# Optimization experiments

Hardware: AMD Instinct MI355X
Metric: run time of the kernel (lower is better)

Reference implementation:

```python
import jax, jax.numpy as jnp
import numpy as np

N_IN, D_IN, N_OUT, D_OUT = 1152, 8, 10, 16
ROUTINGS, NUM_BG = 3, 1
C, H, W = 1, 28, 28
BATCH = 128
DEC_IN = N_OUT * D_OUT  # 160, projection_type=None -> dec_feature_size = outcaps_size


def squash(x, axis=-1):
    norm = jnp.linalg.norm(x, axis=axis, keepdims=True)
    scale = norm ** 2 / (1.0 + norm ** 2) / (norm + 1e-8)
    return scale * x


def scale_coef(x, num_bg):
    # x: [B, n_out] or [B, n_out, n_in]; min/max normalize over dim 1,
    # excluding the last num_bg (background) capsules, then floor at 0.5.
    if num_bg > 0:
        xm = x[:, : x.shape[1] - num_bg]
    else:
        xm = x
    mn = jnp.min(xm, axis=1, keepdims=True)
    mx = jnp.max(xm, axis=1, keepdims=True)
    out = (xm - mn) / jnp.maximum(mx - mn, 1e-6)  # vrange (0,1)
    if num_bg > 0:
        out = jnp.concatenate([out, jnp.zeros_like(out[:, :num_bg])], axis=1)
    return jnp.maximum(out, 0.5)


def decode(capsflat, W1, b1, W2, b2, W3, b3):
    # fcn decoder (eval mode: dropout is identity): 160 -> 512 -> 1024 -> C*H*W
    h = jax.nn.relu(capsflat @ W1 + b1)
    h = jax.nn.relu(h @ W2 + b2)
    return jax.nn.sigmoid(h @ W3 + b3)


def setup_inputs() -> dict:
    key = jax.random.key(0)
    ks = jax.random.split(key, 9)
    return {
        'incaps': jax.random.normal(ks[0], (BATCH, N_IN, D_IN), jnp.float32),
        'x_input': jax.random.uniform(ks[1], (BATCH, C, H, W), jnp.float32),
        'weight': 0.1 * jax.random.normal(ks[2], (N_OUT, N_IN, D_OUT, D_IN), jnp.float32),
        'W1': 0.05 * jax.random.normal(ks[3], (DEC_IN, 512), jnp.float32),
        'b1': jnp.zeros((512,), jnp.float32),
        'W2': 0.05 * jax.random.normal(ks[4], (512, 1024), jnp.float32),
        'b2': jnp.zeros((1024,), jnp.float32),
        'W3': 0.05 * jax.random.normal(ks[5], (1024, C * H * W), jnp.float32),
        'b3': jnp.zeros((C * H * W,), jnp.float32),
    }


def reference(incaps, x_input, weight, W1, b1, W2, b2, W3, b3):
    B = incaps.shape[0]
    # outcaps_hat: matmul(weight, incaps[:,None,:,:,None]).squeeze(-1)
    hat = jnp.einsum('nkoi,bki->bnko', weight, incaps)  # [B, n_out, n_in, d_out]
    hat_d = jax.lax.stop_gradient(hat)
    rc = jnp.ones((B, N_OUT, N_IN), hat.dtype)
    eye = jnp.eye(N_OUT, dtype=hat.dtype)
    x_flat = x_input.reshape(B, 1, -1)
    for _ in range(ROUTINGS - 1):
        # squash over capsule dim, weighted sum over input capsules
        outcaps = squash(jnp.sum(rc[..., None] * hat_d, axis=2, keepdims=True))  # [B,n,1,d]
        b = jnp.sum(outcaps * hat_d, axis=-1)  # agreement [B, n_out, n_in]
        c = scale_coef(b, NUM_BG)
        objcaps = outcaps[:, :, 0, :]  # [B, n_out, d_out]
        # get_every_obj_rscore vectorized: mask one object capsule at a time
        masked = objcaps[:, None, :, :] * eye[None, :, :, None]  # [B, n_obj, n_out, d]
        recon = decode(masked.reshape(B, N_OUT, DEC_IN), W1, b1, W2, b2, W3, b3)  # [B,n_obj,CHW]
        rscore = -jnp.sum((x_flat - recon) ** 2, axis=-1)  # neg MSE-sum, [B, n_obj]
        r = scale_coef(rscore, NUM_BG)
        rc = c * r[:, :, None]
    # final iteration uses non-detached hat
    outcaps = squash(jnp.sum(rc[..., None] * hat, axis=2, keepdims=True))
    return outcaps[:, :, 0, :]  # [B, n_out, d_out]
```

## Files before the change

kernel.cpp:

```cpp
#include <hip/hip_runtime.h>
#include <math.h>

#define BATCH  128
#define NIN    1152
#define DIN    8
#define NOUTC  10
#define DOUT   16
#define H1DIM  512
#define H2DIM  1024
#define PIX    784
#define NROWS  (BATCH * NOUTC)
#define NBY3   13

typedef __attribute__((ext_vector_type(8))) __bf16 bf16x8;
typedef __attribute__((ext_vector_type(4))) float  f32x4;
typedef __attribute__((ext_vector_type(4))) unsigned int u32x4;

__device__ __forceinline__ float bf2f(unsigned int u) {
    union { unsigned int i; float f; } v; v.i = u << 16; return v.f;
}
__device__ __forceinline__ ushort f2bf(float f) {
    union { float f; unsigned int i; } v; v.f = f;
    unsigned int r = v.i + 0x7FFFu + ((v.i >> 16) & 1u);
    return (ushort)(r >> 16);
}
__device__ __forceinline__ float ldin(const void* p, size_t i, int isbf) {
    return isbf ? bf2f(((const ushort*)p)[i]) : ((const float*)p)[i];
}
__device__ __forceinline__ bf16x8 frag_of(uint4 u) {
    return __builtin_bit_cast(bf16x8, u);
}
__device__ __forceinline__ bf16x8 ld_frag(const ushort* p) {
    return frag_of(*(const uint4*)p);
}
__device__ __forceinline__ float dot8(uint4 a, uint4 b) {
    float s;
    s  = bf2f(a.x & 0xffffu) * bf2f(b.x & 0xffffu);
    s += bf2f(a.x >> 16)     * bf2f(b.x >> 16);
    s += bf2f(a.y & 0xffffu) * bf2f(b.y & 0xffffu);
    s += bf2f(a.y >> 16)     * bf2f(b.y >> 16);
    s += bf2f(a.z & 0xffffu) * bf2f(b.z & 0xffffu);
    s += bf2f(a.z >> 16)     * bf2f(b.z >> 16);
    s += bf2f(a.w & 0xffffu) * bf2f(b.w & 0xffffu);
    s += bf2f(a.w >> 16)     * bf2f(b.w >> 16);
    return s;
}
__device__ __forceinline__ uint4 pack8(float4 a, float4 b) {
    uint4 r;
    r.x = f2bf(a.x) | ((unsigned)f2bf(a.y) << 16);
    r.y = f2bf(a.z) | ((unsigned)f2bf(a.w) << 16);
    r.z = f2bf(b.x) | ((unsigned)f2bf(b.y) << 16);
    r.w = f2bf(b.z) | ((unsigned)f2bf(b.w) << 16);
    return r;
}

__device__ __forceinline__ int detect_bf(const void* w, int* cntS) {
    int tid = threadIdx.x, nt = blockDim.x;
    if (tid == 0) *cntS = 0;
    __syncthreads();
    const ushort* u = (const ushort*)w;
    int c = 0;
    for (int s = tid; s < 512; s += nt) {
        int e = (u[s * 2] >> 7) & 0xFF;
        if (e >= 88 && e <= 140) c++;
    }
    atomicAdd(cntS, c);
    __syncthreads();
    return (*cntS >= 384) ? 1 : 0;
}

struct PrepArgs {
    const void* w;
    const void* src[7];
    ushort*     dst[7];
    int         n[7];
    int*        flag;
};

__global__ __launch_bounds__(256) void prep_kernel(PrepArgs a)
{
    __shared__ int cntS;
    __shared__ ushort tile[32][33];
    int tid = threadIdx.x;
    int isbf = detect_bf(a.w, &cntS);
    int seg = blockIdx.y;
    if (seg == 0 && blockIdx.x == 0 && tid == 0) *a.flag = isbf;

    if (seg <= 4) {
        int n = a.n[seg];
        int stride = gridDim.x * 256;
        ushort* d = a.dst[seg];
        if (isbf) {
            const ushort* s = (const ushort*)a.src[seg];
            for (int i = blockIdx.x * 256 + tid; i < n; i += stride) d[i] = s[i];
        } else {
            const float* s = (const float*)a.src[seg];
            for (int i = blockIdx.x * 256 + tid; i < n; i += stride) d[i] = f2bf(s[i]);
        }
        return;
    }
    int R = (seg == 5) ? H1DIM : H2DIM;
    int C = (seg == 5) ? H2DIM : PIX;
    int tilesX = (seg == 5) ? 32 : 25;
    int tilesY = (seg == 5) ? 16 : 32;
    int t = blockIdx.x;
    if (t >= tilesX * tilesY) return;
    int tx2 = t % tilesX, ty2 = t / tilesX;
    int c0 = tx2 * 32, r0 = ty2 * 32;
    const void* in = a.src[seg];
    ushort* out = a.dst[seg];
    int tx = tid & 31, ty = tid >> 5;
    for (int i = ty; i < 32; i += 8) {
        int r = r0 + i, c = c0 + tx;
        tile[i][tx] = (r < R && c < C) ? f2bf(ldin(in, (size_t)r * C + c, isbf)) : (ushort)0;
    }
    __syncthreads();
    for (int i = ty; i < 32; i += 8) {
        int c = c0 + i, r = r0 + tx;
        if (c < C && r < R) out[(size_t)c * R + r] = tile[tx][i];
    }
}

__global__ __launch_bounds__(256) void hat_build(
    const void* __restrict__ inc,
    const void* __restrict__ w,
    ushort* __restrict__ hatG)
{
    __shared__ int cntS;
    int isbf = detect_bf(w, &cntS);
    int kc = blockIdx.x, bc = blockIdx.y, n = blockIdx.z;
    int t  = threadIdx.x;
    int k  = kc * 128 + (t >> 1);
    int oh = (t & 1) << 3;

    size_t wbase = ((size_t)n * NIN + k) * DOUT + oh;
    uint4 wr[8];
    if (isbf) {
        const uint4* wp = (const uint4*)((const ushort*)w + wbase * DIN);
        #pragma unroll
        for (int j = 0; j < 8; j++) wr[j] = wp[j];
    } else {
        const float4* wp = (const float4*)((const float*)w + wbase * DIN);
        #pragma unroll
        for (int j = 0; j < 8; j++) wr[j] = pack8(wp[2 * j], wp[2 * j + 1]);
    }

    int b0 = bc * 16;
    #pragma unroll 4
    for (int bl = 0; bl < 16; bl++) {
        int b = b0 + bl;
        size_t ioff = ((size_t)b * NIN + k) * DIN;
        uint4 iu;
        if (isbf) iu = *(const uint4*)((const ushort*)inc + ioff);
        else {
            const float4* ip = (const float4*)((const float*)inc + ioff);
            iu = pack8(ip[0], ip[1]);
        }
        unsigned int h[8];
        #pragma unroll
        for (int j = 0; j < 8; j++) h[j] = f2bf(dot8(wr[j], iu));
        u32x4 ov = { h[0] | (h[1] << 16), h[2] | (h[3] << 16),
                     h[4] | (h[5] << 16), h[6] | (h[7] << 16) };
        __builtin_nontemporal_store(ov,
            (u32x4*)(hatG + (((size_t)(b * NOUTC + n) * NIN + k) * DOUT + oh)));
    }
}

template<bool COMPUTE>
__global__ __launch_bounds__(512, 4) void reduce_pass(
    const ushort* __restrict__ hatG,
    const void*   __restrict__ incRaw,
    const void*   __restrict__ wRaw,
    const ushort* __restrict__ bsPrev,
    const float*  __restrict__ partials,
    int iter0,
    const ushort* __restrict__ W1c,
    const ushort* __restrict__ b1c,
    ushort* __restrict__ h1out,
    ushort* __restrict__ bsOut,
    void*   __restrict__ outFinal,
    const int* __restrict__ flagp)
{
    int bn  = blockIdx.x;
    int n   = bn % NOUTC;
    int b   = bn / NOUTC;
    int tid = threadIdx.x;

    __shared__ ushort wSb[NIN];
    __shared__ float  redS[8][16];
    __shared__ float  sumS[16];
    __shared__ float  ocS[16];
    __shared__ float  scaleS;

    int h = tid & 1, kb = tid >> 1;
    int wave = tid >> 6, lane = tid & 63;

    uint4 v[4];
    const ushort* tailS;

    if constexpr (!COMPUTE) {
        __shared__ uint4 hatTail4[256];
        const ushort* hbase = hatG + (size_t)bn * NIN * DOUT;
        #pragma unroll
        for (int j = 0; j < 4; j++)
            v[j] = *(const uint4*)(hbase + ((kb + 256 * j) * DOUT + h * 8));
        if (tid < 256)
            hatTail4[tid] = *(const uint4*)(hbase + 1024 * DOUT + tid * 8);
        tailS = (const ushort*)hatTail4;
    } else {
        __shared__ int cntS;
        __shared__ uint4 hatS4[NIN * DOUT / 8];
        int isbf = detect_bf(wRaw, &cntS);
        size_t wnb = (size_t)n * NIN * DOUT * DIN;
        for (int idx = tid; idx < NIN * DOUT; idx += 512) {
            int k = idx >> 4;
            float s = 0.f;
            #pragma unroll
            for (int i = 0; i < 8; i++)
                s += ldin(wRaw, wnb + (size_t)idx * 8 + i, isbf) *
                     ldin(incRaw, ((size_t)b * NIN + k) * DIN + i, isbf);
            ((ushort*)hatS4)[idx] = f2bf(s);
        }
        __syncthreads();
        const ushort* hbase = (const ushort*)hatS4;
        #pragma unroll
        for (int j = 0; j < 4; j++)
            v[j] = *(const uint4*)(hbase + ((kb + 256 * j) * DOUT + h * 8));
        tailS = hbase + 1024 * DOUT;
    }

    if (!iter0) {
        if (tid < 9) {
            float s = 0.f;
            #pragma unroll
            for (int j = 0; j < NBY3; j++)
                s += partials[(size_t)(b * NOUTC + tid) * 16 + j];
            sumS[tid] = -s;
        }
        __syncthreads();
        float mn = 1e30f, mx = -1e30f;
        #pragma unroll
        for (int n2 = 0; n2 < 9; n2++) {
            float vv = sumS[n2];
            mn = fminf(mn, vv); mx = fmaxf(mx, vv);
        }
        float den = fmaxf(mx - mn, 1e-6f);
        float rv = (n < 9) ? fmaxf((sumS[n] - mn) / den, 0.5f) : 0.5f;
        for (int k = tid; k < NIN; k += 512) {
            float c = 0.5f;
            if (n < 9) {
                float vv[9], mn2 = 1e30f, mx2 = -1e30f;
                #pragma unroll
                for (int n2 = 0; n2 < 9; n2++) {
                    vv[n2] = bf2f(bsPrev[(size_t)(b * NOUTC + n2) * NIN + k]);
                    mn2 = fminf(mn2, vv[n2]); mx2 = fmaxf(mx2, vv[n2]);
                }
                float den2 = fmaxf(mx2 - mn2, 1e-6f);
                c = fmaxf((vv[n] - mn2) / den2, 0.5f);
            }
            wSb[k] = f2bf(c * rv);
        }
    }
    __syncthreads();

    float acc[8];
    #pragma unroll
    for (int o = 0; o < 8; o++) acc[o] = 0.f;
    #pragma unroll
    for (int j = 0; j < 4; j++) {
        int k = kb + 256 * j;
        float w = iter0 ? 1.f : bf2f(wSb[k]);
        bf16x8 hv = frag_of(v[j]);
        #pragma unroll
        for (int o = 0; o < 8; o++) acc[o] += w * (float)hv[o];
    }
    if (tid < 256) {
        int k = 1024 + kb;
        float w = iter0 ? 1.f : bf2f(wSb[k]);
        bf16x8 hv = ld_frag(tailS + kb * DOUT + h * 8);
        #pragma unroll
        for (int o = 0; o < 8; o++) acc[o] += w * (float)hv[o];
    }
    #pragma unroll
    for (int off = 32; off >= 2; off >>= 1) {
        #pragma unroll
        for (int o = 0; o < 8; o++) acc[o] += __shfl_xor(acc[o], off);
    }
    if (lane < 2) {
        #pragma unroll
        for (int o = 0; o < 8; o++) redS[wave][lane * 8 + o] = acc[o];
    }
    __syncthreads();
    if (tid < 16) {
        float s = 0.f;
        #pragma unroll
        for (int wv = 0; wv < 8; wv++) s += redS[wv][tid];
        sumS[tid] = s;
    }
    __syncthreads();
    if (tid == 0) {
        float n2 = 0.f;
        #pragma unroll
        for (int o = 0; o < 16; o++) n2 += sumS[o] * sumS[o];
        float nrm = sqrtf(n2);
        scaleS = n2 / (1.f + n2) / (nrm + 1e-8f);
    }
    __syncthreads();
    if (tid < 16) {
        float oc = scaleS * sumS[tid];
        ocS[tid] = oc;
        if (outFinal) {
            if (*flagp) ((ushort*)outFinal)[(size_t)bn * 16 + tid] = f2bf(oc);
            else        ((float*) outFinal)[(size_t)bn * 16 + tid] = oc;
        }
    }
    __syncthreads();

    if (bsOut) {
        float o0 = ocS[h * 8 + 0], o1 = ocS[h * 8 + 1], o2 = ocS[h * 8 + 2],
              o3 = ocS[h * 8 + 3], o4 = ocS[h * 8 + 4], o5 = ocS[h * 8 + 5],
              o6 = ocS[h * 8 + 6], o7 = ocS[h * 8 + 7];
        #pragma unroll
        for (int j = 0; j < 4; j++) {
            bf16x8 hv = frag_of(v[j]);
            float s = o0 * (float)hv[0] + o1 * (float)hv[1] + o2 * (float)hv[2] +
                      o3 * (float)hv[3] + o4 * (float)hv[4] + o5 * (float)hv[5] +
                      o6 * (float)hv[6] + o7 * (float)hv[7];
            s += __shfl_xor(s, 1);
            if (h == 0) bsOut[(size_t)bn * NIN + kb + 256 * j] = f2bf(s);
        }
        if (tid < 256) {
            bf16x8 hv = ld_frag(tailS + kb * DOUT + h * 8);
            float s = o0 * (float)hv[0] + o1 * (float)hv[1] + o2 * (float)hv[2] +
                      o3 * (float)hv[3] + o4 * (float)hv[4] + o5 * (float)hv[5] +
                      o6 * (float)hv[6] + o7 * (float)hv[7];
            s += __shfl_xor(s, 1);
            if (h == 0) bsOut[(size_t)bn * NIN + 1024 + kb] = f2bf(s);
        }
    }

    if (h1out) {
        int col = tid;
        float acc1 = bf2f(b1c[col]);
        #pragma unroll
        for (int i = 0; i < 16; i++)
            acc1 += ocS[i] * bf2f(W1c[(size_t)(n * 16 + i) * H1DIM + col]);
        h1out[(size_t)bn * H1DIM + col] = f2bf(fmaxf(acc1, 0.f));
    }
}

__global__ __launch_bounds__(256) void gemm_kernel(
    const ushort* __restrict__ A, const ushort* __restrict__ Bt,
    const ushort* __restrict__ bias, int K, int N,
    ushort* __restrict__ Cout,
    const ushort* __restrict__ xin, float* __restrict__ partials)
{
    int m0 = blockIdx.x * 64, n0 = blockIdx.y * 64;
    int tid = threadIdx.x;
    int wave = tid >> 6, lane = tid & 63, quad = lane >> 4, l16 = lane & 15;

    __shared__ uint4 As4[320];
    __shared__ uint4 Bs4[320];
    ushort* As = (ushort*)As4;
    ushort* Bs = (ushort*)Bs4;

    f32x4 acc[4];
    #pragma unroll
    for (int nt = 0; nt < 4; nt++)
        #pragma unroll
        for (int rg = 0; rg < 4; rg++) acc[nt][rg] = 0.f;

    int sMi = tid >> 2, sKk = (tid & 3) * 8;
    int sLds = sMi * 5 + (tid & 3);
    const ushort* Ap = A + (size_t)(m0 + sMi) * K + sKk;
    const ushort* Bp = Bt + (size_t)(n0 + sMi) * K + sKk;
    bool bOK = (n0 + sMi) < N;

    uint4 aR = *(const uint4*)Ap;
    uint4 bR = bOK ? *(const uint4*)Bp : make_uint4(0, 0, 0, 0);

    for (int k0 = 0; k0 < K; k0 += 32) {
        As4[sLds] = aR;
        Bs4[sLds] = bR;
        __syncthreads();
        if (k0 + 32 < K) {
            aR = *(const uint4*)(Ap + k0 + 32);
            bR = bOK ? *(const uint4*)(Bp + k0 + 32) : make_uint4(0, 0, 0, 0);
        }
        bf16x8 a = ld_frag(As + (wave * 16 + l16) * 40 + quad * 8);
        #pragma unroll
        for (int nt = 0; nt < 4; nt++) {
            bf16x8 bb = ld_frag(Bs + (nt * 16 + l16) * 40 + quad * 8);
            acc[nt] = __builtin_amdgcn_mfma_f32_16x16x32_bf16(a, bb, acc[nt], 0, 0, 0);
        }
        __syncthreads();
    }

    int rowBase = m0 + wave * 16 + quad * 4;
    if (Cout) {
        #pragma unroll
        for (int nt = 0; nt < 4; nt++) {
            int col = n0 + nt * 16 + l16;
            float bv = bf2f(bias[col]);
            #pragma unroll
            for (int rg = 0; rg < 4; rg++) {
                float v = acc[nt][rg] + bv;
                Cout[(size_t)(rowBase + rg) * N + col] = f2bf(fmaxf(v, 0.f));
            }
        }
    } else {
        float vr[4] = {0.f, 0.f, 0.f, 0.f};
        #pragma unroll
        for (int nt = 0; nt < 4; nt++) {
            int col = n0 + nt * 16 + l16;
            if (col < N) {
                float bv = bf2f(bias[col]);
                #pragma unroll
                for (int rg = 0; rg < 4; rg++) {
                    int row = rowBase + rg;
                    int bb = row / NOUTC;
                    float z = acc[nt][rg] + bv;
                    float s = 1.f / (1.f + __expf(-z));
                    float d = bf2f(xin[(size_t)bb * PIX + col]) - s;
                    vr[rg] += d * d;
                }
            }
        }
        #pragma unroll
        for (int rg = 0; rg < 4; rg++) {
            float v = vr[rg];
            #pragma unroll
            for (int off = 8; off >= 1; off >>= 1) v += __shfl_xor(v, off, 16);
            if (l16 == 0)
                partials[(size_t)(rowBase + rg) * 16 + blockIdx.y] = v;
        }
    }
}

extern "C" void kernel_launch(void* const* d_in, const int* in_sizes, int n_in,
                              void* d_out, int out_size, void* d_ws, size_t ws_size,
                              hipStream_t stream)
{
    const void* inc = d_in[0];
    const void* x   = d_in[1];
    const void* w   = d_in[2];
    const void* W1  = d_in[3];
    const void* b1  = d_in[4];
    const void* W2  = d_in[5];
    const void* b2  = d_in[6];
    const void* W3  = d_in[7];
    const void* b3  = d_in[8];

    char* p = (char*)d_ws;
    auto alloc = [&](size_t bytes) { void* r = p; p += (bytes + 255) & ~(size_t)255; return r; };
    int*    flagWS    = (int*)alloc(256);
    ushort* bsA       = (ushort*)alloc((size_t)NROWS * NIN * 2);
    ushort* bsB       = (ushort*)alloc((size_t)NROWS * NIN * 2);
    float*  partials  = (float*)alloc((size_t)NROWS * 16 * 4);
    ushort* h1WS      = (ushort*)alloc((size_t)NROWS * H1DIM * 2);
    ushort* h2WS      = (ushort*)alloc((size_t)NROWS * H2DIM * 2);
    ushort* W2T       = (ushort*)alloc((size_t)H2DIM * H1DIM * 2);
    ushort* W3T       = (ushort*)alloc((size_t)PIX * H2DIM * 2);
    ushort* W1c       = (ushort*)alloc((size_t)160 * H1DIM * 2);
    ushort* b1c       = (ushort*)alloc((size_t)H1DIM * 2);
    ushort* b2c       = (ushort*)alloc((size_t)H2DIM * 2);
    ushort* b3c       = (ushort*)alloc((size_t)PIX * 2);
    ushort* xc        = (ushort*)alloc((size_t)BATCH * PIX * 2);
    ushort* hatG      = (ushort*)alloc((size_t)NROWS * NIN * DOUT * 2);
    bool haveHat = ((char*)hatG + (size_t)NROWS * NIN * DOUT * 2) <= ((char*)d_ws + ws_size);

    PrepArgs pa;
    pa.w = w;
    pa.src[0] = W1;  pa.dst[0] = W1c;  pa.n[0] = 160 * H1DIM;
    pa.src[1] = b1;  pa.dst[1] = b1c;  pa.n[1] = H1DIM;
    pa.src[2] = b2;  pa.dst[2] = b2c;  pa.n[2] = H2DIM;
    pa.src[3] = b3;  pa.dst[3] = b3c;  pa.n[3] = PIX;
    pa.src[4] = x;   pa.dst[4] = xc;   pa.n[4] = BATCH * PIX;
    pa.src[5] = W2;  pa.dst[5] = W2T;  pa.n[5] = 0;
    pa.src[6] = W3;  pa.dst[6] = W3T;  pa.n[6] = 0;
    pa.flag = flagWS;
    prep_kernel<<<dim3(800, 7), 256, 0, stream>>>(pa);

    if (haveHat) hat_build<<<dim3(9, 8, NOUTC), 256, 0, stream>>>(inc, w, hatG);

    if (haveHat)
        reduce_pass<false><<<NROWS, 512, 0, stream>>>(
            hatG, inc, w, nullptr, nullptr, 1,
            W1c, b1c, h1WS, bsA, nullptr, flagWS);
    else
        reduce_pass<true><<<NROWS, 512, 0, stream>>>(
            nullptr, inc, w, nullptr, nullptr, 1,
            W1c, b1c, h1WS, bsA, nullptr, flagWS);

    for (int it = 0; it < 2; it++) {
        gemm_kernel<<<dim3(NROWS / 64, H2DIM / 64), 256, 0, stream>>>(
            h1WS, W2T, b2c, H1DIM, H2DIM, h2WS, nullptr, nullptr);
        gemm_kernel<<<dim3(NROWS / 64, NBY3), 256, 0, stream>>>(
            h2WS, W3T, b3c, H2DIM, PIX, nullptr, xc, partials);

        int last = (it == 1);
        const ushort* bsP = (it == 0) ? bsA : bsB;
        ushort* bsO       = last ? nullptr : bsB;
        ushort* h1o       = last ? nullptr : h1WS;
        void*   fin       = last ? d_out : nullptr;
        if (haveHat)
            reduce_pass<false><<<NROWS, 512, 0, stream>>>(
                hatG, inc, w, bsP, partials, 0,
                W1c, b1c, h1o, bsO, fin, flagWS);
        else
            reduce_pass<true><<<NROWS, 512, 0, stream>>>(
                nullptr, inc, w, bsP, partials, 0,
                W1c, b1c, h1o, bsO, fin, flagWS);
    }
}
```

Baseline: 214.1 us.

## Fuse weight prep into hat build, use fp32 hat math, double GEMM k-step

Merges the separate prep kernel into the hat-building kernel by appending extra grid slices that perform the weight transposes, bias/input conversions and flag write, which removes one kernel launch. The hat computation now unpacks weights and inputs to fp32 once instead of re-converting bf16 in every dot product. The GEMM stages two 32-wide k-chunks per barrier pair to halve synchronisation, at the cost of doubling shared memory. The 96 transpose blocks each loop over about 14 tiles, which may lengthen the critical path of the fused kernel.

```diff
diff --git a/kernel.cpp b/kernel.cpp
--- a/kernel.cpp
+++ b/kernel.cpp
@@ -33,17 +33,11 @@
 __device__ __forceinline__ bf16x8 ld_frag(const ushort* p) {
     return frag_of(*(const uint4*)p);
 }
-__device__ __forceinline__ float dot8(uint4 a, uint4 b) {
-    float s;
-    s  = bf2f(a.x & 0xffffu) * bf2f(b.x & 0xffffu);
-    s += bf2f(a.x >> 16)     * bf2f(b.x >> 16);
-    s += bf2f(a.y & 0xffffu) * bf2f(b.y & 0xffffu);
-    s += bf2f(a.y >> 16)     * bf2f(b.y >> 16);
-    s += bf2f(a.z & 0xffffu) * bf2f(b.z & 0xffffu);
-    s += bf2f(a.z >> 16)     * bf2f(b.z >> 16);
-    s += bf2f(a.w & 0xffffu) * bf2f(b.w & 0xffffu);
-    s += bf2f(a.w >> 16)     * bf2f(b.w >> 16);
-    return s;
+__device__ __forceinline__ void unpack8(uint4 u, float* f) {
+    f[0] = bf2f(u.x & 0xffffu); f[1] = bf2f(u.x >> 16);
+    f[2] = bf2f(u.y & 0xffffu); f[3] = bf2f(u.y >> 16);
+    f[4] = bf2f(u.z & 0xffffu); f[5] = bf2f(u.z >> 16);
+    f[6] = bf2f(u.w & 0xffffu); f[7] = bf2f(u.w >> 16);
 }
 __device__ __forceinline__ uint4 pack8(float4 a, float4 b) {
     uint4 r;
@@ -121,44 +115,104 @@
     }
 }
 
-__global__ __launch_bounds__(256) void hat_build(
+__global__ __launch_bounds__(256) void hat_prep_kernel(
     const void* __restrict__ inc,
-    const void* __restrict__ w,
+    PrepArgs a,
     ushort* __restrict__ hatG)
 {
     __shared__ int cntS;
-    int isbf = detect_bf(w, &cntS);
+    __shared__ ushort tile[32][33];
+    int tid = threadIdx.x;
+    int isbf = detect_bf(a.w, &cntS);
+
+    if (blockIdx.z >= NOUTC) {
+        int p = (blockIdx.z - NOUTC) * 72 + blockIdx.y * 9 + blockIdx.x;
+        if (p == 0 && tid == 0) *a.flag = isbf;
+        if (p < 96) {
+            for (int t = p; t < 1312; t += 96) {
+                int seg = (t < 512) ? 5 : 6;
+                int tt  = (seg == 5) ? t : t - 512;
+                int R = (seg == 5) ? H1DIM : H2DIM;
+                int C = (seg == 5) ? H2DIM : PIX;
+                int tilesX = (seg == 5) ? 32 : 25;
+                int tx2 = tt % tilesX, ty2 = tt / tilesX;
+                int c0 = tx2 * 32, r0 = ty2 * 32;
+                const void* in = a.src[seg];
+                ushort* out = a.dst[seg];
+                int tx = tid & 31, ty = tid >> 5;
+                for (int i = ty; i < 32; i += 8) {
+                    int r = r0 + i, c = c0 + tx;
+                    tile[i][tx] = (r < R && c < C) ? f2bf(ldin(in, (size_t)r * C + c, isbf)) : (ushort)0;
+                }
+                __syncthreads();
+                for (int i = ty; i < 32; i += 8) {
+                    int c = c0 + i, r = r0 + tx;
+                    if (c < C && r < R) out[(size_t)c * R + r] = tile[tx][i];
+                }
+                __syncthreads();
+            }
+        } else {
+            int base = (p - 96) * 256 + tid;
+            const int stride = 48 * 256;
+            #pragma unroll
+            for (int seg = 0; seg <= 4; seg++) {
+                int n = a.n[seg];
+                ushort* d = a.dst[seg];
+                if (isbf) {
+                    const ushort* s = (const ushort*)a.src[seg];
+                    for (int i = base; i < n; i += stride) d[i] = s[i];
+                } else {
+                    const float* s = (const float*)a.src[seg];
+                    for (int i = base; i < n; i += stride) d[i] = f2bf(s[i]);
+                }
+            }
+        }
+        return;
+    }
+
     int kc = blockIdx.x, bc = blockIdx.y, n = blockIdx.z;
-    int t  = threadIdx.x;
-    int k  = kc * 128 + (t >> 1);
-    int oh = (t & 1) << 3;
+    int k  = kc * 128 + (tid >> 1);
+    int oh = (tid & 1) << 3;
 
     size_t wbase = ((size_t)n * NIN + k) * DOUT + oh;
-    uint4 wr[8];
+    float wf[8][8];
     if (isbf) {
-        const uint4* wp = (const uint4*)((const ushort*)w + wbase * DIN);
-        #pragma unroll
-        for (int j = 0; j < 8; j++) wr[j] = wp[j];
+        const uint4* wp = (const uint4*)((const ushort*)a.w + wbase * DIN);
+        #pragma unroll
+        for (int j = 0; j < 8; j++) unpack8(wp[j], wf[j]);
     } else {
-        const float4* wp = (const float4*)((const float*)w + wbase * DIN);
-        #pragma unroll
-        for (int j = 0; j < 8; j++) wr[j] = pack8(wp[2 * j], wp[2 * j + 1]);
+        const float4* wp = (const float4*)((const float*)a.w + wbase * DIN);
+        #pragma unroll
+        for (int j = 0; j < 8; j++) {
+            float4 lo = wp[2 * j], hi = wp[2 * j + 1];
+            wf[j][0] = lo.x; wf[j][1] = lo.y; wf[j][2] = lo.z; wf[j][3] = lo.w;
+            wf[j][4] = hi.x; wf[j][5] = hi.y; wf[j][6] = hi.z; wf[j][7] = hi.w;
+        }
     }
 
     int b0 = bc * 16;
-    #pragma unroll 4
+    #pragma unroll 2
     for (int bl = 0; bl < 16; bl++) {
         int b = b0 + bl;
         size_t ioff = ((size_t)b * NIN + k) * DIN;
-        uint4 iu;
-        if (isbf) iu = *(const uint4*)((const ushort*)inc + ioff);
-        else {
+        float xi[8];
+        if (isbf) {
+            uint4 iu = *(const uint4*)((const ushort*)inc + ioff);
+            unpack8(iu, xi);
+        } else {
             const float4* ip = (const float4*)((const float*)inc + ioff);
-            iu = pack8(ip[0], ip[1]);
+            float4 lo = ip[0], hi = ip[1];
+            xi[0] = lo.x; xi[1] = lo.y; xi[2] = lo.z; xi[3] = lo.w;
+            xi[4] = hi.x; xi[5] = hi.y; xi[6] = hi.z; xi[7] = hi.w;
         }
         unsigned int h[8];
         #pragma unroll
-        for (int j = 0; j < 8; j++) h[j] = f2bf(dot8(wr[j], iu));
+        for (int j = 0; j < 8; j++) {
+            float s = wf[j][0] * xi[0] + wf[j][1] * xi[1] + wf[j][2] * xi[2] +
+                      wf[j][3] * xi[3] + wf[j][4] * xi[4] + wf[j][5] * xi[5] +
+                      wf[j][6] * xi[6] + wf[j][7] * xi[7];
+            h[j] = f2bf(s);
+        }
         u32x4 ov = { h[0] | (h[1] << 16), h[2] | (h[3] << 16),
                      h[4] | (h[5] << 16), h[6] | (h[7] << 16) };
         __builtin_nontemporal_store(ov,
@@ -359,8 +413,8 @@
     int tid = threadIdx.x;
     int wave = tid >> 6, lane = tid & 63, quad = lane >> 4, l16 = lane & 15;
 
-    __shared__ uint4 As4[320];
-    __shared__ uint4 Bs4[320];
+    __shared__ uint4 As4[640];
+    __shared__ uint4 Bs4[640];
     ushort* As = (ushort*)As4;
     ushort* Bs = (ushort*)Bs4;
 
@@ -376,22 +430,31 @@
     const ushort* Bp = Bt + (size_t)(n0 + sMi) * K + sKk;
     bool bOK = (n0 + sMi) < N;
 
-    uint4 aR = *(const uint4*)Ap;
-    uint4 bR = bOK ? *(const uint4*)Bp : make_uint4(0, 0, 0, 0);
-
-    for (int k0 = 0; k0 < K; k0 += 32) {
-        As4[sLds] = aR;
-        Bs4[sLds] = bR;
+    uint4 aR0 = *(const uint4*)Ap;
+    uint4 aR1 = *(const uint4*)(Ap + 32);
+    uint4 bR0 = bOK ? *(const uint4*)Bp : make_uint4(0, 0, 0, 0);
+    uint4 bR1 = bOK ? *(const uint4*)(Bp + 32) : make_uint4(0, 0, 0, 0);
+
+    for (int k0 = 0; k0 < K; k0 += 64) {
+        As4[sLds]       = aR0;
+        As4[320 + sLds] = aR1;
+        Bs4[sLds]       = bR0;
+        Bs4[320 + sLds] = bR1;
         __syncthreads();
-        if (k0 + 32 < K) {
-            aR = *(const uint4*)(Ap + k0 + 32);
-            bR = bOK ? *(const uint4*)(Bp + k0 + 32) : make_uint4(0, 0, 0, 0);
-        }
-        bf16x8 a = ld_frag(As + (wave * 16 + l16) * 40 + quad * 8);
-        #pragma unroll
-        for (int nt = 0; nt < 4; nt++) {
-            bf16x8 bb = ld_frag(Bs + (nt * 16 + l16) * 40 + quad * 8);
-            acc[nt] = __builtin_amdgcn_mfma_f32_16x16x32_bf16(a, bb, acc[nt], 0, 0, 0);
+        if (k0 + 64 < K) {
+            aR0 = *(const uint4*)(Ap + k0 + 64);
+            aR1 = *(const uint4*)(Ap + k0 + 96);
+            bR0 = bOK ? *(const uint4*)(Bp + k0 + 64) : make_uint4(0, 0, 0, 0);
+            bR1 = bOK ? *(const uint4*)(Bp + k0 + 96) : make_uint4(0, 0, 0, 0);
+        }
+        #pragma unroll
+        for (int c = 0; c < 2; c++) {
+            bf16x8 a = ld_frag(As + c * 2560 + (wave * 16 + l16) * 40 + quad * 8);
+            #pragma unroll
+            for (int nt = 0; nt < 4; nt++) {
+                bf16x8 bb = ld_frag(Bs + c * 2560 + (nt * 16 + l16) * 40 + quad * 8);
+                acc[nt] = __builtin_amdgcn_mfma_f32_16x16x32_bf16(a, bb, acc[nt], 0, 0, 0);
+            }
         }
         __syncthreads();
     }
@@ -479,9 +542,12 @@
     pa.src[5] = W2;  pa.dst[5] = W2T;  pa.n[5] = 0;
     pa.src[6] = W3;  pa.dst[6] = W3T;  pa.n[6] = 0;
     pa.flag = flagWS;
-    prep_kernel<<<dim3(800, 7), 256, 0, stream>>>(pa);
-
-    if (haveHat) hat_build<<<dim3(9, 8, NOUTC), 256, 0, stream>>>(inc, w, hatG);
+
+    if (haveHat) {
+        hat_prep_kernel<<<dim3(9, 8, NOUTC + 2), 256, 0, stream>>>(inc, pa, hatG);
+    } else {
+        prep_kernel<<<dim3(800, 7), 256, 0, stream>>>(pa);
+    }
 
     if (haveHat)
         reduce_pass<false><<<NROWS, 512, 0, stream>>>(
```

New measurement: 207.3 us. -3.2%, faster.
